# Optimization experiments

Measured on AMD Instinct MI355X. Metric: run time of the kernel, lower is better.

Reference implementation:

```python
import jax, jax.numpy as jnp
import numpy as np
from jax import lax

NMS_TH = 0.05
TOPK_P = 1000
NMS_IOU = 0.5
NUMDETS = 100
NMS_ITERS = 15
IM = 2048.0
SIZES = [256, 128, 64, 32, 16]
NUM_CLASS = 80


def _make_boxes(key, n):
    k1, k2, k3, k4 = jax.random.split(key, 4)
    cy = jax.random.uniform(k1, (n,)) * IM
    cx = jax.random.uniform(k2, (n,)) * IM
    h = jax.random.uniform(k3, (n,)) * 300.0 + 16.0
    w = jax.random.uniform(k4, (n,)) * 300.0 + 16.0
    # yxyx boxes
    return jnp.stack([cy - h / 2, cx - w / 2, cy + h / 2, cx + w / 2], axis=1)


def setup_inputs() -> dict:
    key = jax.random.key(0)
    inp = {}
    for s, sz in enumerate(SIZES):
        kc = jax.random.fold_in(key, 2 * s)
        kb = jax.random.fold_in(key, 2 * s + 1)
        n = sz * sz
        inp['cls%d' % s] = jax.random.normal(kc, (1, n, NUM_CLASS), jnp.float32) - 2.0
        inp['reg%d' % s] = _make_boxes(kb, n)[None]
    inp['locations'] = jnp.array([0.0, 0.0, IM - 1.0, IM - 1.0, 1024.0, 1024.0], jnp.float32)
    return inp


def _pairwise_iou(a, b):
    # a: (N,4) yxyx, b: (M,4) yxyx -> (N,M)
    area_a = jnp.clip(a[:, 2] - a[:, 0], 0) * jnp.clip(a[:, 3] - a[:, 1], 0)
    area_b = jnp.clip(b[:, 2] - b[:, 0], 0) * jnp.clip(b[:, 3] - b[:, 1], 0)
    iy1 = jnp.maximum(a[:, None, 0], b[None, :, 0])
    ix1 = jnp.maximum(a[:, None, 1], b[None, :, 1])
    iy2 = jnp.minimum(a[:, None, 2], b[None, :, 2])
    ix2 = jnp.minimum(a[:, None, 3], b[None, :, 3])
    inter = jnp.clip(iy2 - iy1, 0) * jnp.clip(ix2 - ix1, 0)
    union = area_a[:, None] + area_b[None, :] - inter
    return inter / jnp.maximum(union, 1e-9)


def _cluster_nms(boxes, scores, classes, valid, iou_th):
    order = jnp.argsort(-scores)
    b = boxes[order]
    s = scores[order]
    c = classes[order]
    v = valid[order]
    iou = jnp.triu(_pairwise_iou(b, b), k=1)  # (K,K)

    def body(B, _):
        max_a = B.max(axis=0)
        keep_col = (max_a <= iou_th).astype(B.dtype)[:, None]
        return iou * keep_col, None

    B, _ = lax.scan(body, iou, None, length=NMS_ITERS)
    keep = (B.max(axis=0) <= iou_th) & v
    return b, s, c, keep


def _per_level(cls_s, reg_s):
    p = jax.nn.sigmoid(cls_s[0])                 # (N, C)
    ps = p.max(axis=1)                           # (N,)
    pi = p.argmax(axis=1).astype(jnp.int32) + 1  # class index, 0 is background
    m = ps > NMS_TH
    ps_m = jnp.where(m, ps, -1.0)
    k = min(TOPK_P, ps_m.shape[0])
    top_s, top_idx = lax.top_k(ps_m, k)
    return top_s, pi[top_idx], reg_s[0][top_idx], m[top_idx]


def reference(cls0, cls1, cls2, cls3, cls4, reg0, reg1, reg2, reg3, reg4, locations):
    levels = [(cls0, reg0), (cls1, reg1), (cls2, reg2), (cls3, reg3), (cls4, reg4)]
    sc, cl, bx, vd = [], [], [], []
    for cls_s, reg_s in levels:
        s_, c_, b_, v_ = _per_level(cls_s, reg_s)
        sc.append(s_); cl.append(c_); bx.append(b_); vd.append(v_)
    scores = jnp.concatenate(sc)
    classes = jnp.concatenate(cl)
    boxes = jnp.concatenate(bx, axis=0)
    valid = jnp.concatenate(vd)
    scores = jnp.where(valid, scores, 0.0)

    vy1, vx1, vy2, vx2 = locations[0], locations[1], locations[2], locations[3]
    ori_h, ori_w = locations[4], locations[5]
    boxes = jnp.stack([
        jnp.maximum(boxes[:, 0], vy1), jnp.maximum(boxes[:, 1], vx1),
        jnp.minimum(boxes[:, 2], vy2), jnp.minimum(boxes[:, 3], vx2)], axis=1)

    b, s, c, keep = _cluster_nms(boxes, scores, classes, valid, NMS_IOU)
    s = jnp.where(keep, s, 0.0)
    top_s, sel = lax.top_k(s, NUMDETS)
    bbox = b[sel]
    cls_out = c[sel]

    # transfer boxes back to original-image coordinates
    sy = ori_h / jnp.maximum(vy2 - vy1, 1e-6)
    sx = ori_w / jnp.maximum(vx2 - vx1, 1e-6)
    bbox = jnp.stack([
        (bbox[:, 0] - vy1) * sy, (bbox[:, 1] - vx1) * sx,
        (bbox[:, 2] - vy1) * sy, (bbox[:, 3] - vx1) * sx], axis=1)
    return bbox, cls_out, top_s
```

## Files before the change

### kernel.cpp

```cpp
#include <hip/hip_runtime.h>
#include <math.h>


#define NANCH 87296
#define NF 4256
#define CAPD 128
#define NITER 16
#define BCAP 512
#define EC 8192
#define NBLK 341
#define BASE20 0xBD4CCu
#define NB20 9216
#define BPT 9

struct InPtrs {
    const float* cls[5];
    const float* reg[5];
    const float* loc;
};

constexpr size_t SZ_HIST  = 5ull * NB20 * 4;
constexpr size_t OFF_HIST = 0;
constexpr size_t OFF_CNT  = OFF_HIST + SZ_HIST;
constexpr size_t OFF_CTR  = OFF_CNT + (size_t)NF * 4;
constexpr size_t ZERO_SZ  = OFF_CTR + 128;
constexpr size_t OFF_SBITS = ((ZERO_SZ + 255) / 256) * 256;
constexpr size_t OFF_CLSV  = OFF_SBITS + (size_t)NANCH * 4;
constexpr size_t OFF_PAR   = OFF_CLSV + (size_t)NANCH * 4;
constexpr size_t OFF_INVB  = OFF_PAR + 128;
constexpr size_t OFF_INVO  = OFF_INVB + (size_t)NBLK * 4;
constexpr size_t OFF_FINK  = ((OFF_INVO + (size_t)NBLK * 4 + 255) / 256) * 256;
constexpr size_t OFF_BBUF  = OFF_FINK + (size_t)NF * 8;
constexpr size_t OFF_SBOX  = OFF_BBUF + 5ull * BCAP * 8;
constexpr size_t OFF_SSC   = OFF_SBOX + (size_t)NF * 16;
constexpr size_t OFF_SCV   = OFF_SSC + (size_t)NF * 4;
constexpr size_t OFF_SAR   = OFF_SCV + (size_t)NF * 4;
constexpr size_t OFF_NBR   = OFF_SAR + (size_t)NF * 4;

__device__ __forceinline__ void lvl_of(int a, int& lev, int& idx) {
    if (a < 65536)      { lev = 0; idx = a; }
    else if (a < 81920) { lev = 1; idx = a - 65536; }
    else if (a < 86016) { lev = 2; idx = a - 81920; }
    else if (a < 87040) { lev = 3; idx = a - 86016; }
    else                { lev = 4; idx = a - 87040; }
}

__device__ __forceinline__ unsigned int fkey(float f) {
    unsigned int u = __float_as_uint(f);
    return u ^ ((u & 0x80000000u) ? 0xFFFFFFFFu : 0x80000000u);
}
__device__ __forceinline__ float funkey(unsigned int k) {
    return __uint_as_float(k ^ ((k & 0x80000000u) ? 0x80000000u : 0xFFFFFFFFu));
}
__device__ __forceinline__ unsigned int bin20_addr(unsigned int v) {
    unsigned int owner = v / BPT;
    unsigned int i = v - owner * BPT;
    return (i << 10) | owner;
}
__device__ __forceinline__ unsigned int ald(const unsigned int* p) {
    return __hip_atomic_load((unsigned int*)p, __ATOMIC_RELAXED, __HIP_MEMORY_SCOPE_AGENT);
}
__device__ __forceinline__ void ast64(unsigned long long* p, unsigned long long v) {
    __hip_atomic_store(p, v, __ATOMIC_RELAXED, __HIP_MEMORY_SCOPE_AGENT);
}
__device__ __forceinline__ unsigned long long ald64(const unsigned long long* p) {
    return __hip_atomic_load((unsigned long long*)p, __ATOMIC_RELAXED, __HIP_MEMORY_SCOPE_AGENT);
}

__global__ __launch_bounds__(1024) void k1_score(InPtrs P, unsigned int* hist,
        unsigned int* sbits, unsigned int* clsv, unsigned int* invBlk) {
    int t = threadIdx.x;
    int a = blockIdx.x * 256 + (t >> 2);
    int k = t & 3;
    int lev, idx; lvl_of(a, lev, idx);
    const float4* row = (const float4*)(P.cls[lev] + (size_t)idx * 80);
    float4 v[5];
    #pragma unroll
    for (int q = 0; q < 5; ++q) v[q] = row[q * 4 + k];
    float best = -INFINITY; int bi = 0;
    #pragma unroll
    for (int q = 0; q < 5; ++q) {
        int c0 = q * 16 + k * 4;
        if (v[q].x > best) { best = v[q].x; bi = c0 + 0; }
        if (v[q].y > best) { best = v[q].y; bi = c0 + 1; }
        if (v[q].z > best) { best = v[q].z; bi = c0 + 2; }
        if (v[q].w > best) { best = v[q].w; bi = c0 + 3; }
    }
    #pragma unroll
    for (int m = 1; m < 4; m <<= 1) {
        float ob = __shfl_xor(best, m, 64);
        int  obi = __shfl_xor(bi, m, 64);
        if (ob > best || (ob == best && obi < bi)) { best = ob; bi = obi; }
    }
    bool lead = (k == 0);
    unsigned int valid = 0;
    if (lead) {
        float score = 1.0f / (1.0f + expf(-best));
        valid = (score > 0.05f) ? 1u : 0u;
        float psm = valid ? score : -1.0f;
        unsigned int sb = fkey(psm);
        sbits[a] = sb;
        clsv[a] = (unsigned int)(bi + 1) | (valid << 31);
        if (valid) {
            unsigned int bin = (sb >> 12) - BASE20;
            atomicAdd(&hist[(size_t)lev * NB20 + bin20_addr(bin)], 1u);
        }
    }
    __shared__ unsigned int wv[16];
    unsigned long long mv = __ballot(lead && valid);
    int lane = t & 63, w = t >> 6;
    if (lane == 0) wv[w] = (unsigned int)__popcll(mv);
    __syncthreads();
    if (t == 0) {
        unsigned int s = 0;
        #pragma unroll
        for (int i = 0; i < 16; ++i) s += wv[i];
        invBlk[blockIdx.x] = 256u - s;
    }
}

__global__ __launch_bounds__(1024) void k2_scan(const unsigned int* hist,
        const unsigned int* invBlk, unsigned int* params, unsigned int* invOff) {
    int t = threadIdx.x;
    if (blockIdx.x == 5) {
        __shared__ unsigned int sv[512];
        __shared__ unsigned int orig[512];
        if (t < 512) {
            unsigned int v = (t < NBLK) ? invBlk[t] : 0u;
            sv[t] = v; orig[t] = v;
        }
        __syncthreads();
        for (int off = 1; off < 512; off <<= 1) {
            unsigned int add = 0;
            if (t < 512 && t >= off) add = sv[t - off];
            __syncthreads();
            if (t < 512) sv[t] += add;
            __syncthreads();
        }
        if (t < NBLK) {
            int segStart = (t < 256) ? 0 : (t < 320) ? 256 : (t < 336) ? 320
                         : (t < 340) ? 336 : 340;
            invOff[t] = sv[t] - orig[t] - (segStart > 0 ? sv[segStart - 1] : 0u);
        }
        return;
    }
    int lev = blockIdx.x;
    unsigned int K = (lev == 4) ? 256u : 1000u;
    const unsigned int* h = hist + (size_t)lev * NB20;
    __shared__ unsigned int seg[1024];
    __shared__ unsigned int suf[1024];
    unsigned int hc[BPT];
    unsigned int s = 0;
    #pragma unroll
    for (int i = 0; i < BPT; ++i) { hc[i] = h[(i << 10) | t]; s += hc[i]; }
    seg[t] = s;
    suf[t] = s;
    __syncthreads();
    for (int off = 1; off < 1024; off <<= 1) {
        unsigned int v = suf[t];
        unsigned int add = (t + off < 1024) ? suf[t + off] : 0u;
        __syncthreads();
        suf[t] = v + add;
        __syncthreads();
    }
    unsigned int totValid = suf[0];
    if (totValid >= K) {
        unsigned int excl = suf[t] - seg[t];
        if (excl < K && excl + seg[t] >= K) {
            unsigned int cum = excl;
            for (int i = BPT - 1; i >= 0; --i) {
                unsigned int c = hc[i];
                if (cum + c >= K) {
                    params[lev] = (unsigned int)(t * BPT + i);
                    params[8 + lev] = K - cum;
                    params[16 + lev] = 0;
                    break;
                }
                cum += c;
            }
        }
    } else if (t == 0) {
        params[lev] = 0;
        params[8 + lev] = 0;
        params[16 + lev] = K - totValid;
    }
}

__global__ __launch_bounds__(256) void k3_compact(const unsigned int* sbits,
        const unsigned int* clsv, const unsigned int* params,
        const unsigned int* invOff, unsigned long long* finKeys,
        unsigned int* ctrs, unsigned long long* bBuf) {
    int blk = blockIdx.x;
    int t = threadIdx.x;
    int a = blk * 256 + t;
    int lev, idx; lvl_of(a, lev, idx);
    unsigned int sb = sbits[a];
    unsigned int cv = clsv[a];
    unsigned int bin = (sb >> 12) - BASE20;
    unsigned int Bs = params[lev];
    unsigned int rNeg = params[16 + lev];
    unsigned int valid = cv >> 31;
    int lane = t & 63, w = t >> 6;
    unsigned long long lt = (1ull << lane) - 1ull;
    __shared__ unsigned int wInv[4], wFin[4], wB[4];
    __shared__ unsigned int baseFin, baseB;
    unsigned long long mInv = __ballot(valid == 0u);
    if (lane == 0) wInv[w] = (unsigned int)__popcll(mInv);
    __syncthreads();
    unsigned int invRank = invOff[blk] + (unsigned int)__popcll(mInv & lt);
    for (int i = 0; i < w; ++i) invRank += wInv[i];
    bool isFin, isB;
    if (valid) {
        isFin = (bin > Bs);
        isB   = (bin == Bs);
    } else {
        isFin = (rNeg > 0) && (invRank < rNeg);
        isB   = false;
    }
    unsigned long long mFin = __ballot(isFin);
    unsigned long long mB   = __ballot(isB);
    if (lane == 0) { wFin[w] = (unsigned int)__popcll(mFin); wB[w] = (unsigned int)__popcll(mB); }
    __syncthreads();
    if (t == 0) {
        unsigned int tf = wFin[0] + wFin[1] + wFin[2] + wFin[3];
        unsigned int tb = wB[0] + wB[1] + wB[2] + wB[3];
        baseFin = tf ? atomicAdd(&ctrs[0], tf) : 0u;
        baseB   = tb ? atomicAdd(&ctrs[1 + lev], tb) : 0u;
    }
    __syncthreads();
    if (isFin || isB) {
        unsigned int composite = ((unsigned int)lev << 16) | (unsigned int)idx;
        unsigned int inv = (~composite) & 0x7FFFFu;
        unsigned int low = (inv << 13) | (valid << 7) | (cv & 0x7Fu);
        unsigned long long key = ((unsigned long long)sb << 32) | low;
        if (isFin) {
            unsigned int p = baseFin + (unsigned int)__popcll(mFin & lt);
            for (int i = 0; i < w; ++i) p += wFin[i];
            if (p < NF) finKeys[p] = key;
        } else {
            unsigned int p = baseB + (unsigned int)__popcll(mB & lt);
            for (int i = 0; i < w; ++i) p += wB[i];
            if (p < BCAP) ast64(&bBuf[(size_t)lev * BCAP + p], key);
        }
    }
    __shared__ unsigned int isLast;
    __shared__ unsigned long long kb[BCAP];
    __shared__ unsigned int posS;
    __syncthreads();
    if (t == 0) {
        asm volatile("s_waitcnt vmcnt(0)" ::: "memory");
        unsigned int r = __hip_atomic_fetch_add(&ctrs[8], 1u,
                             __ATOMIC_RELAXED, __HIP_MEMORY_SCOPE_AGENT);
        isLast = (r == (unsigned int)(NBLK - 1)) ? 1u : 0u;
    }
    __syncthreads();
    if (!isLast) return;
    unsigned int fc = ald(&ctrs[0]);
    if (fc > NF) fc = NF;
    if (t == 0) posS = fc;
    __syncthreads();
    for (int blev = 0; blev < 5; ++blev) {
        unsigned int bc = ald(&ctrs[1 + blev]);
        int n = (bc > BCAP) ? BCAP : (int)bc;
        int r = (int)params[8 + blev];
        if (r > n) r = n;
        if (r > 0) {
            for (int i = t; i < n; i += 256)
                kb[i] = ald64(&bBuf[(size_t)blev * BCAP + i]);
            __syncthreads();
            for (int i = t; i < n; i += 256) {
                unsigned long long my = kb[i];
                unsigned int c = 0;
                for (int j = 0; j < n; ++j) c += (kb[j] > my) ? 1u : 0u;
                if (c < (unsigned int)r) {
                    unsigned int p = atomicAdd(&posS, 1u);
                    if (p < NF) finKeys[p] = my;
                }
            }
            __syncthreads();
        }
    }
    for (int i = (int)posS + t; i < NF; i += 256)
        finKeys[i] = (unsigned long long)i;
}

__global__ __launch_bounds__(1024) void k5_rank(InPtrs P,
        const unsigned long long* finKeys,
        float4* sBox, float* sScore, unsigned int* sCV, float* sArea) {
    __shared__ __align__(16) unsigned long long keys[NF];
    __shared__ unsigned int rnk[64];
    int t = threadIdx.x;
    {
        const ulonglong2* src = (const ulonglong2*)finKeys;
        ulonglong2* dst = (ulonglong2*)keys;
        for (int i = t; i < NF / 2; i += 1024) dst[i] = src[i];
    }
    if (t < 64) rnk[t] = 0;
    __syncthreads();
    int lf = t & 63;
    int seg = t >> 6;
    int f = blockIdx.x * 64 + lf;
    unsigned long long my = (f < NF) ? keys[f] : 0ull;
    if (f < NF) {
        unsigned int c = 0;
        const ulonglong2* kp = (const ulonglong2*)keys + seg * 133;
        #pragma unroll 4
        for (int i = 0; i < 133; ++i) {
            ulonglong2 v = kp[i];
            c += (v.x > my) ? 1u : 0u;
            c += (v.y > my) ? 1u : 0u;
        }
        atomicAdd(&rnk[lf], c);
    }
    __syncthreads();
    if (seg == 0 && f < NF) {
        unsigned int r = rnk[lf];
        unsigned int sb  = (unsigned int)(my >> 32);
        unsigned int low = (unsigned int)my;
        unsigned int composite = (~(low >> 13)) & 0x7FFFFu;
        int lev = composite >> 16;
        int idx = composite & 0xFFFF;
        float4 b = ((const float4*)P.reg[lev])[idx];
        float vy1 = P.loc[0], vx1 = P.loc[1], vy2 = P.loc[2], vx2 = P.loc[3];
        float y1 = fmaxf(b.x, vy1), x1 = fmaxf(b.y, vx1);
        float y2 = fminf(b.z, vy2), x2 = fminf(b.w, vx2);
        float area = __fmul_rn(fmaxf(y2 - y1, 0.0f), fmaxf(x2 - x1, 0.0f));
        unsigned int valid = (low >> 7) & 1u;
        sBox[r] = make_float4(y1, x1, y2, x2);
        sScore[r] = valid ? funkey(sb) : 0.0f;
        sCV[r] = (low & 0x7Fu) | (valid << 31);
        sArea[r] = area;
    }
}

__global__ __launch_bounds__(256) void k6_adj(const float4* sBox,
        const float* sArea, unsigned int* cnt, unsigned short* nbr) {
    int L = blockIdx.x;
    float fr = sqrtf(8.0f * (float)L + 1.0f);
    int jt = (int)((fr - 1.0f) * 0.5f);
    while ((jt + 1) * (jt + 2) / 2 <= L) jt++;
    while (jt * (jt + 1) / 2 > L) jt--;
    int it = L - jt * (jt + 1) / 2;
    __shared__ float4 cb[64]; __shared__ float ca[64];
    __shared__ float4 rb[64]; __shared__ float ra[64];
    int t = threadIdx.x;
    if (t < 64) {
        int j = jt * 64 + t;
        if (j < NF) { cb[t] = sBox[j]; ca[t] = sArea[j]; }
        int i = it * 64 + t;
        if (i < NF) { rb[t] = sBox[i]; ra[t] = sArea[i]; }
    }
    __syncthreads();
    int lj = t & 63;
    int j = jt * 64 + lj;
    if (j >= NF) return;
    float4 B = cb[lj]; float ab = ca[lj];
    for (int li = (t >> 6); li < 64; li += 4) {
        int i = it * 64 + li;
        if (i >= j) continue;
        float4 A = rb[li]; float aa = ra[li];
        float iy1 = fmaxf(A.x, B.x), ix1 = fmaxf(A.y, B.y);
        float iy2 = fminf(A.z, B.z), ix2 = fminf(A.w, B.w);
        float ih = fmaxf(iy2 - iy1, 0.0f), iw = fmaxf(ix2 - ix1, 0.0f);
        float inter = __fmul_rn(ih, iw);
        float uni = __fsub_rn(__fadd_rn(aa, ab), inter);
        float iou = __fdiv_rn(inter, fmaxf(uni, 1e-9f));
        if (iou > 0.5f) {
            unsigned int p = atomicAdd(&cnt[j], 1u);
            if (p < CAPD) nbr[(size_t)j * CAPD + p] = (unsigned short)i;
        }
    }
}

__global__ __launch_bounds__(1024) void k7_nms(InPtrs P, const float4* sBox,
        const float* sScore, const unsigned int* sCV, const unsigned int* cnt,
        const unsigned short* nbr, float* out) {
    __shared__ unsigned int edges[EC];
    __shared__ __align__(4) unsigned char bufA[NF];
    __shared__ __align__(4) unsigned char bufB[NF];
    __shared__ unsigned int wsum[16];
    __shared__ float ploc[6];
    __shared__ unsigned int chg;
    int t = threadIdx.x;
    int lane = t & 63, wid = t >> 6;
    if (t < 6) ploc[t] = P.loc[t];
    const int CH = 5;
    unsigned int dq[CH];
    unsigned int s = 0;
    #pragma unroll
    for (int q = 0; q < CH; ++q) {
        int j = t * CH + q;
        unsigned int d = 0;
        if (j < NF) { d = cnt[j]; if (d > CAPD) d = CAPD; }
        dq[q] = d; s += d;
    }
    unsigned int sc = s;
    #pragma unroll
    for (int o = 1; o < 64; o <<= 1) {
        unsigned int n = __shfl_up(sc, o, 64);
        if (lane >= o) sc += n;
    }
    if (lane == 63) wsum[wid] = sc;
    if (t < 1064) ((unsigned int*)bufA)[t] = 0x01010101u;
    __syncthreads();
    unsigned int wbase = 0, tot = 0;
    #pragma unroll
    for (int i = 0; i < 16; ++i) {
        unsigned int v = wsum[i];
        if (i < wid) wbase += v;
        tot += v;
    }
    unsigned int E = tot;
    bool useLds = (E <= (unsigned int)EC);
    if (useLds) {
        unsigned int base = wbase + sc - s;
        #pragma unroll
        for (int q = 0; q < CH; ++q) {
            int j = t * CH + q;
            if (j < NF) {
                unsigned int d = dq[q];
                const unsigned short* nl = nbr + (size_t)j * CAPD;
                for (unsigned int e = 0; e < d; ++e)
                    edges[base + e] = ((unsigned int)nl[e] << 16) | (unsigned int)j;
                base += d;
            }
        }
    }
    __syncthreads();
    unsigned char* cur = bufA; unsigned char* nxt = bufB;
    for (int itr = 0; itr < NITER; ++itr) {
        if (t < 1064) ((unsigned int*)nxt)[t] = 0x01010101u;
        __syncthreads();
        if (useLds) {
            for (int e = t; e < (int)E; e += 1024) {
                unsigned int pk = edges[e];
                if (cur[pk >> 16]) nxt[pk & 0xFFFFu] = 0;
            }
        } else {
            for (int j = t; j < NF; j += 1024) {
                unsigned int d = cnt[j]; if (d > CAPD) d = CAPD;
                const unsigned short* nl = nbr + (size_t)j * CAPD;
                unsigned int hit = 0;
                for (unsigned int e = 0; e < d; ++e)
                    hit |= (unsigned int)cur[nl[e]];
                if (hit) nxt[j] = 0;
            }
        }
        __syncthreads();
        if (t < 1064 &&
            ((unsigned int*)nxt)[t] != ((unsigned int*)cur)[t]) chg = 1;
        __syncthreads();
        unsigned int done = (chg == 0u);
        unsigned char* tm = cur; cur = nxt; nxt = tm;
        __syncthreads();
        if (t == 0) chg = 0;
        if (done) break;
    }
    int base = t * CH;
    unsigned char kf[CH];
    unsigned int sum = 0;
    #pragma unroll
    for (int q = 0; q < CH; ++q) {
        int j = base + q;
        unsigned char v = 0;
        if (j < NF) v = cur[j] & (unsigned char)(sCV[j] >> 31);
        kf[q] = v; sum += v;
    }
    unsigned int sc2 = sum;
    #pragma unroll
    for (int o = 1; o < 64; o <<= 1) {
        unsigned int n = __shfl_up(sc2, o, 64);
        if (lane >= o) sc2 += n;
    }
    if (lane == 63) wsum[wid] = sc2;
    __syncthreads();
    unsigned int wbase2 = 0, keptTot = 0;
    #pragma unroll
    for (int i = 0; i < 16; ++i) {
        unsigned int v = wsum[i];
        if (i < wid) wbase2 += v;
        keptTot += v;
    }
    unsigned int run = wbase2 + sc2 - sum;
    float vy1 = ploc[0], vx1 = ploc[1], vy2 = ploc[2], vx2 = ploc[3];
    float sy = ploc[4] / fmaxf(vy2 - vy1, 1e-6f);
    float sx = ploc[5] / fmaxf(vx2 - vx1, 1e-6f);
    #pragma unroll
    for (int q = 0; q < CH; ++q) {
        int j = base + q;
        if (j >= NF) break;
        unsigned int slot = 0xFFFFFFFFu;
        float scv = 0.0f;
        if (kf[q]) {
            if (run < 100u) { slot = run; scv = sScore[j]; }
            run++;
        } else if (keptTot < 100u) {
            unsigned int nk = (unsigned int)j - run;
            unsigned int s2 = keptTot + nk;
            if (s2 < 100u) { slot = s2; scv = 0.0f; }
        }
        if (slot < 100u) {
            float4 b = sBox[j];
            out[slot * 4 + 0] = (b.x - vy1) * sy;
            out[slot * 4 + 1] = (b.y - vx1) * sx;
            out[slot * 4 + 2] = (b.z - vy1) * sy;
            out[slot * 4 + 3] = (b.w - vx1) * sx;
            out[400 + slot] = (float)(sCV[j] & 0x7Fu);
            out[500 + slot] = scv;
        }
    }
}

extern "C" void kernel_launch(void* const* d_in, const int* in_sizes, int n_in,
                              void* d_out, int out_size, void* d_ws, size_t ws_size,
                              hipStream_t stream) {
    (void)n_in; (void)out_size; (void)ws_size;
    InPtrs P;
    bool inter = (in_sizes[1] == 65536 * 4);
    for (int s = 0; s < 5; ++s) {
        P.cls[s] = (const float*)d_in[inter ? 2 * s : s];
        P.reg[s] = (const float*)d_in[inter ? 2 * s + 1 : 5 + s];
    }
    P.loc = (const float*)d_in[10];

    char* w = (char*)d_ws;
    unsigned int* hist   = (unsigned int*)(w + OFF_HIST);
    unsigned int* cnt    = (unsigned int*)(w + OFF_CNT);
    unsigned int* ctrs   = (unsigned int*)(w + OFF_CTR);
    unsigned int* sbits  = (unsigned int*)(w + OFF_SBITS);
    unsigned int* clsv   = (unsigned int*)(w + OFF_CLSV);
    unsigned int* params = (unsigned int*)(w + OFF_PAR);
    unsigned int* invBlk = (unsigned int*)(w + OFF_INVB);
    unsigned int* invOff = (unsigned int*)(w + OFF_INVO);
    unsigned long long* finKeys = (unsigned long long*)(w + OFF_FINK);
    unsigned long long* bBuf    = (unsigned long long*)(w + OFF_BBUF);
    float4* sBox  = (float4*)(w + OFF_SBOX);
    float* sScore = (float*)(w + OFF_SSC);
    unsigned int* sCV = (unsigned int*)(w + OFF_SCV);
    float* sArea  = (float*)(w + OFF_SAR);
    unsigned short* nbr = (unsigned short*)(w + OFF_NBR);

    hipMemsetAsync(d_ws, 0, ZERO_SZ, stream);
    k1_score<<<NBLK, 1024, 0, stream>>>(P, hist, sbits, clsv, invBlk);
    k2_scan<<<6, 1024, 0, stream>>>(hist, invBlk, params, invOff);
    k3_compact<<<NBLK, 256, 0, stream>>>(sbits, clsv, params, invOff, finKeys, ctrs, bBuf);
    k5_rank<<<67, 1024, 0, stream>>>(P, finKeys, sBox, sScore, sCV, sArea);
    k6_adj<<<2278, 256, 0, stream>>>(sBox, sArea, cnt, nbr);
    k7_nms<<<1, 1024, 0, stream>>>(P, sBox, sScore, sCV, cnt, nbr, (float*)d_out);
}
```

Measured before the change: 173.0 us.

## Fuse scan into score kernel and rank into compact kernel via last-block patterns

Removes two kernel launches. The histogram threshold scan and invalid-offset scan now run in the last block to finish k1_score, found with an atomic counter. The rank stage is folded into the compact kernel: the last 67 blocks to arrive spin-wait on a flag set by the final block after it has merged the boundary-bin keys, then each computes ranks with 256 threads instead of 1024. This cuts launch gaps but makes blocks busy-wait inside the grid and narrows the rank parallelism per block.

Result: slower. 192.0 us (+11.0%).

```diff
diff --git a/kernel.cpp b/kernel.cpp
--- a/kernel.cpp
+++ b/kernel.cpp
@@ -12,6 +12,7 @@
 #define BASE20 0xBD4CCu
 #define NB20 9216
 #define BPT 9
+#define NRANK 67
 
 struct InPtrs {
     const float* cls[5];
@@ -60,6 +61,9 @@
 __device__ __forceinline__ unsigned int ald(const unsigned int* p) {
     return __hip_atomic_load((unsigned int*)p, __ATOMIC_RELAXED, __HIP_MEMORY_SCOPE_AGENT);
 }
+__device__ __forceinline__ void ast(unsigned int* p, unsigned int v) {
+    __hip_atomic_store(p, v, __ATOMIC_RELAXED, __HIP_MEMORY_SCOPE_AGENT);
+}
 __device__ __forceinline__ void ast64(unsigned long long* p, unsigned long long v) {
     __hip_atomic_store(p, v, __ATOMIC_RELAXED, __HIP_MEMORY_SCOPE_AGENT);
 }
@@ -68,7 +72,8 @@
 }
 
 __global__ __launch_bounds__(1024) void k1_score(InPtrs P, unsigned int* hist,
-        unsigned int* sbits, unsigned int* clsv, unsigned int* invBlk) {
+        unsigned int* sbits, unsigned int* clsv, unsigned int* invBlk,
+        unsigned int* params, unsigned int* invOff, unsigned int* ctrs) {
     int t = threadIdx.x;
     int a = blockIdx.x * 256 + (t >> 2);
     int k = t & 3;
@@ -107,6 +112,7 @@
         }
     }
     __shared__ unsigned int wv[16];
+    __shared__ unsigned int isLast;
     unsigned long long mv = __ballot(lead && valid);
     int lane = t & 63, w = t >> 6;
     if (lane == 0) wv[w] = (unsigned int)__popcll(mv);
@@ -115,81 +121,91 @@
         unsigned int s = 0;
         #pragma unroll
         for (int i = 0; i < 16; ++i) s += wv[i];
-        invBlk[blockIdx.x] = 256u - s;
-    }
-}
-
-__global__ __launch_bounds__(1024) void k2_scan(const unsigned int* hist,
-        const unsigned int* invBlk, unsigned int* params, unsigned int* invOff) {
-    int t = threadIdx.x;
-    if (blockIdx.x == 5) {
-        __shared__ unsigned int sv[512];
-        __shared__ unsigned int orig[512];
-        if (t < 512) {
-            unsigned int v = (t < NBLK) ? invBlk[t] : 0u;
-            sv[t] = v; orig[t] = v;
-        }
-        __syncthreads();
-        for (int off = 1; off < 512; off <<= 1) {
-            unsigned int add = 0;
-            if (t < 512 && t >= off) add = sv[t - off];
-            __syncthreads();
-            if (t < 512) sv[t] += add;
-            __syncthreads();
-        }
-        if (t < NBLK) {
-            int segStart = (t < 256) ? 0 : (t < 320) ? 256 : (t < 336) ? 320
-                         : (t < 340) ? 336 : 340;
-            invOff[t] = sv[t] - orig[t] - (segStart > 0 ? sv[segStart - 1] : 0u);
-        }
-        return;
-    }
-    int lev = blockIdx.x;
-    unsigned int K = (lev == 4) ? 256u : 1000u;
-    const unsigned int* h = hist + (size_t)lev * NB20;
-    __shared__ unsigned int seg[1024];
-    __shared__ unsigned int suf[1024];
-    unsigned int hc[BPT];
-    unsigned int s = 0;
-    #pragma unroll
-    for (int i = 0; i < BPT; ++i) { hc[i] = h[(i << 10) | t]; s += hc[i]; }
-    seg[t] = s;
-    suf[t] = s;
+        ast(&invBlk[blockIdx.x], 256u - s);
+    }
+    __syncthreads();
+    if (t == 0) {
+        asm volatile("s_waitcnt vmcnt(0)" ::: "memory");
+        unsigned int r = __hip_atomic_fetch_add(&ctrs[11], 1u,
+                             __ATOMIC_RELAXED, __HIP_MEMORY_SCOPE_AGENT);
+        isLast = (r == (unsigned int)(NBLK - 1)) ? 1u : 0u;
+    }
+    __syncthreads();
+    if (!isLast) return;
+
+    __shared__ unsigned int sc[5 * 1024];
+    unsigned int s4[5];
+    #pragma unroll
+    for (int lv = 0; lv < 5; ++lv) {
+        const unsigned int* h = hist + (size_t)lv * NB20;
+        unsigned int s = 0;
+        #pragma unroll
+        for (int i = 0; i < BPT; ++i) s += ald(&h[(i << 10) | t]);
+        s4[lv] = s; sc[lv * 1024 + t] = s;
+    }
     __syncthreads();
     for (int off = 1; off < 1024; off <<= 1) {
-        unsigned int v = suf[t];
-        unsigned int add = (t + off < 1024) ? suf[t + off] : 0u;
-        __syncthreads();
-        suf[t] = v + add;
-        __syncthreads();
-    }
-    unsigned int totValid = suf[0];
-    if (totValid >= K) {
-        unsigned int excl = suf[t] - seg[t];
-        if (excl < K && excl + seg[t] >= K) {
-            unsigned int cum = excl;
-            for (int i = BPT - 1; i >= 0; --i) {
-                unsigned int c = hc[i];
-                if (cum + c >= K) {
-                    params[lev] = (unsigned int)(t * BPT + i);
-                    params[8 + lev] = K - cum;
-                    params[16 + lev] = 0;
-                    break;
+        unsigned int vv[5], a2[5];
+        #pragma unroll
+        for (int lv = 0; lv < 5; ++lv) {
+            vv[lv] = sc[lv * 1024 + t];
+            a2[lv] = (t + off < 1024) ? sc[lv * 1024 + t + off] : 0u;
+        }
+        __syncthreads();
+        #pragma unroll
+        for (int lv = 0; lv < 5; ++lv) sc[lv * 1024 + t] = vv[lv] + a2[lv];
+        __syncthreads();
+    }
+    #pragma unroll
+    for (int lv = 0; lv < 5; ++lv) {
+        unsigned int K = (lv == 4) ? 256u : 1000u;
+        unsigned int tot = sc[lv * 1024];
+        if (tot >= K) {
+            unsigned int suf = sc[lv * 1024 + t];
+            unsigned int excl = suf - s4[lv];
+            if (excl < K && suf >= K) {
+                const unsigned int* h = hist + (size_t)lv * NB20;
+                unsigned int cum = excl;
+                for (int i = BPT - 1; i >= 0; --i) {
+                    unsigned int c = ald(&h[(i << 10) | t]);
+                    if (cum + c >= K) {
+                        params[lv] = (unsigned int)(t * BPT + i);
+                        params[8 + lv] = K - cum;
+                        params[16 + lv] = 0;
+                        break;
+                    }
+                    cum += c;
                 }
-                cum += c;
             }
-        }
-    } else if (t == 0) {
-        params[lev] = 0;
-        params[8 + lev] = 0;
-        params[16 + lev] = K - totValid;
-    }
-}
-
-__global__ __launch_bounds__(256) void k3_compact(const unsigned int* sbits,
-        const unsigned int* clsv, const unsigned int* params,
-        const unsigned int* invOff, unsigned long long* finKeys,
-        unsigned int* ctrs, unsigned long long* bBuf) {
+        } else if (t == 0) {
+            params[lv] = 0; params[8 + lv] = 0; params[16 + lv] = K - tot;
+        }
+    }
+    __syncthreads();
+    if (t < 512) {
+        unsigned int vv = (t < NBLK) ? ald(&invBlk[t]) : 0u;
+        sc[t] = vv; sc[1024 + t] = vv;
+    }
+    __syncthreads();
+    for (int off = 1; off < 512; off <<= 1) {
+        unsigned int add = 0;
+        if (t < 512 && t >= off) add = sc[t - off];
+        __syncthreads();
+        if (t < 512) sc[t] += add;
+        __syncthreads();
+    }
+    if (t < NBLK) {
+        int segStart = (t < 256) ? 0 : (t < 320) ? 256 : (t < 336) ? 320
+                     : (t < 340) ? 336 : 340;
+        invOff[t] = sc[t] - sc[1024 + t] - (segStart > 0 ? sc[segStart - 1] : 0u);
+    }
+}
+
+__global__ __launch_bounds__(256) void k3_rank(InPtrs P,
+        const unsigned int* sbits, const unsigned int* clsv,
+        const unsigned int* params, const unsigned int* invOff,
+        unsigned long long* finKeys, unsigned int* ctrs, unsigned long long* bBuf,
+        float4* sBox, float* sScore, unsigned int* sCV, float* sArea) {
     int blk = blockIdx.x;
     int t = threadIdx.x;
     int a = blk * 256 + t;
@@ -203,23 +219,23 @@
     int lane = t & 63, w = t >> 6;
     unsigned long long lt = (1ull << lane) - 1ull;
     __shared__ unsigned int wInv[4], wFin[4], wB[4];
-    __shared__ unsigned int baseFin, baseB;
+    __shared__ unsigned int baseFin, baseB, myRank, posS;
+    __shared__ union {
+        unsigned long long kb[BCAP];
+        struct { unsigned long long keys[NF]; unsigned int rnk[64]; } rk;
+    } u;
     unsigned long long mInv = __ballot(valid == 0u);
     if (lane == 0) wInv[w] = (unsigned int)__popcll(mInv);
     __syncthreads();
     unsigned int invRank = invOff[blk] + (unsigned int)__popcll(mInv & lt);
     for (int i = 0; i < w; ++i) invRank += wInv[i];
     bool isFin, isB;
-    if (valid) {
-        isFin = (bin > Bs);
-        isB   = (bin == Bs);
-    } else {
-        isFin = (rNeg > 0) && (invRank < rNeg);
-        isB   = false;
-    }
+    if (valid) { isFin = (bin > Bs); isB = (bin == Bs); }
+    else       { isFin = (rNeg > 0) && (invRank < rNeg); isB = false; }
     unsigned long long mFin = __ballot(isFin);
     unsigned long long mB   = __ballot(isB);
-    if (lane == 0) { wFin[w] = (unsigned int)__popcll(mFin); wB[w] = (unsigned int)__popcll(mB); }
+    if (lane == 0) { wFin[w] = (unsigned int)__popcll(mFin);
+                     wB[w]   = (unsigned int)__popcll(mB); }
     __syncthreads();
     if (t == 0) {
         unsigned int tf = wFin[0] + wFin[1] + wFin[2] + wFin[3];
@@ -236,99 +252,97 @@
         if (isFin) {
             unsigned int p = baseFin + (unsigned int)__popcll(mFin & lt);
             for (int i = 0; i < w; ++i) p += wFin[i];
-            if (p < NF) finKeys[p] = key;
+            if (p < NF) ast64(&finKeys[p], key);
         } else {
             unsigned int p = baseB + (unsigned int)__popcll(mB & lt);
             for (int i = 0; i < w; ++i) p += wB[i];
             if (p < BCAP) ast64(&bBuf[(size_t)lev * BCAP + p], key);
         }
     }
-    __shared__ unsigned int isLast;
-    __shared__ unsigned long long kb[BCAP];
-    __shared__ unsigned int posS;
     __syncthreads();
     if (t == 0) {
         asm volatile("s_waitcnt vmcnt(0)" ::: "memory");
-        unsigned int r = __hip_atomic_fetch_add(&ctrs[8], 1u,
-                             __ATOMIC_RELAXED, __HIP_MEMORY_SCOPE_AGENT);
-        isLast = (r == (unsigned int)(NBLK - 1)) ? 1u : 0u;
-    }
-    __syncthreads();
-    if (!isLast) return;
-    unsigned int fc = ald(&ctrs[0]);
-    if (fc > NF) fc = NF;
-    if (t == 0) posS = fc;
-    __syncthreads();
-    for (int blev = 0; blev < 5; ++blev) {
-        unsigned int bc = ald(&ctrs[1 + blev]);
-        int n = (bc > BCAP) ? BCAP : (int)bc;
-        int r = (int)params[8 + blev];
-        if (r > n) r = n;
-        if (r > 0) {
-            for (int i = t; i < n; i += 256)
-                kb[i] = ald64(&bBuf[(size_t)blev * BCAP + i]);
-            __syncthreads();
-            for (int i = t; i < n; i += 256) {
-                unsigned long long my = kb[i];
-                unsigned int c = 0;
-                for (int j = 0; j < n; ++j) c += (kb[j] > my) ? 1u : 0u;
-                if (c < (unsigned int)r) {
-                    unsigned int p = atomicAdd(&posS, 1u);
-                    if (p < NF) finKeys[p] = my;
+        myRank = __hip_atomic_fetch_add(&ctrs[8], 1u,
+                     __ATOMIC_RELAXED, __HIP_MEMORY_SCOPE_AGENT);
+    }
+    __syncthreads();
+    unsigned int rk_ = myRank;
+    if (rk_ < (unsigned int)(NBLK - 1 - NRANK)) return;
+
+    if (rk_ == (unsigned int)(NBLK - 1)) {
+        unsigned int fc = ald(&ctrs[0]);
+        if (fc > NF) fc = NF;
+        if (t == 0) posS = fc;
+        __syncthreads();
+        for (int blev = 0; blev < 5; ++blev) {
+            unsigned int bc = ald(&ctrs[1 + blev]);
+            int n = (bc > BCAP) ? BCAP : (int)bc;
+            int r = (int)params[8 + blev];
+            if (r > n) r = n;
+            if (r > 0) {
+                for (int i = t; i < n; i += 256)
+                    u.kb[i] = ald64(&bBuf[(size_t)blev * BCAP + i]);
+                __syncthreads();
+                for (int i = t; i < n; i += 256) {
+                    unsigned long long my = u.kb[i];
+                    unsigned int c = 0;
+                    for (int j = 0; j < n; ++j) c += (u.kb[j] > my) ? 1u : 0u;
+                    if (c < (unsigned int)r) {
+                        unsigned int p = atomicAdd(&posS, 1u);
+                        if (p < NF) ast64(&finKeys[p], my);
+                    }
                 }
+                __syncthreads();
             }
-            __syncthreads();
-        }
-    }
-    for (int i = (int)posS + t; i < NF; i += 256)
-        finKeys[i] = (unsigned long long)i;
-}
-
-__global__ __launch_bounds__(1024) void k5_rank(InPtrs P,
-        const unsigned long long* finKeys,
-        float4* sBox, float* sScore, unsigned int* sCV, float* sArea) {
-    __shared__ __align__(16) unsigned long long keys[NF];
-    __shared__ unsigned int rnk[64];
-    int t = threadIdx.x;
-    {
-        const ulonglong2* src = (const ulonglong2*)finKeys;
-        ulonglong2* dst = (ulonglong2*)keys;
-        for (int i = t; i < NF / 2; i += 1024) dst[i] = src[i];
-    }
-    if (t < 64) rnk[t] = 0;
+        }
+        __syncthreads();
+        for (int i = (int)posS + t; i < NF; i += 256)
+            ast64(&finKeys[i], (unsigned long long)i);
+        __syncthreads();
+        if (t == 0) {
+            asm volatile("s_waitcnt vmcnt(0)" ::: "memory");
+            ast(&ctrs[10], 1u);
+        }
+        return;
+    }
+
+    if (t == 0) {
+        int g = 0;
+        while (ald(&ctrs[10]) == 0u && g < 200000) { __builtin_amdgcn_s_sleep(8); ++g; }
+    }
+    __syncthreads();
+    int rb = (int)rk_ - (NBLK - 1 - NRANK);
+    for (int i = t; i < NF; i += 256) u.rk.keys[i] = ald64(&finKeys[i]);
+    if (t < 64) u.rk.rnk[t] = 0;
     __syncthreads();
     int lf = t & 63;
     int seg = t >> 6;
-    int f = blockIdx.x * 64 + lf;
-    unsigned long long my = (f < NF) ? keys[f] : 0ull;
+    int f = rb * 64 + lf;
+    unsigned long long my = (f < NF) ? u.rk.keys[f] : 0ull;
     if (f < NF) {
         unsigned int c = 0;
-        const ulonglong2* kp = (const ulonglong2*)keys + seg * 133;
-        #pragma unroll 4
-        for (int i = 0; i < 133; ++i) {
-            ulonglong2 v = kp[i];
-            c += (v.x > my) ? 1u : 0u;
-            c += (v.y > my) ? 1u : 0u;
-        }
-        atomicAdd(&rnk[lf], c);
+        const unsigned long long* kp = u.rk.keys + seg * 1064;
+        #pragma unroll 8
+        for (int i = 0; i < 1064; ++i) c += (kp[i] > my) ? 1u : 0u;
+        atomicAdd(&u.rk.rnk[lf], c);
     }
     __syncthreads();
     if (seg == 0 && f < NF) {
-        unsigned int r = rnk[lf];
-        unsigned int sb  = (unsigned int)(my >> 32);
+        unsigned int r = u.rk.rnk[lf];
+        unsigned int sbv = (unsigned int)(my >> 32);
         unsigned int low = (unsigned int)my;
         unsigned int composite = (~(low >> 13)) & 0x7FFFFu;
-        int lev = composite >> 16;
-        int idx = composite & 0xFFFF;
-        float4 b = ((const float4*)P.reg[lev])[idx];
+        int lev2 = composite >> 16;
+        int idx2 = composite & 0xFFFF;
+        float4 b = ((const float4*)P.reg[lev2])[idx2];
         float vy1 = P.loc[0], vx1 = P.loc[1], vy2 = P.loc[2], vx2 = P.loc[3];
         float y1 = fmaxf(b.x, vy1), x1 = fmaxf(b.y, vx1);
         float y2 = fminf(b.z, vy2), x2 = fminf(b.w, vx2);
         float area = __fmul_rn(fmaxf(y2 - y1, 0.0f), fmaxf(x2 - x1, 0.0f));
-        unsigned int valid = (low >> 7) & 1u;
+        unsigned int valid2 = (low >> 7) & 1u;
         sBox[r] = make_float4(y1, x1, y2, x2);
-        sScore[r] = valid ? funkey(sb) : 0.0f;
-        sCV[r] = (low & 0x7Fu) | (valid << 31);
+        sScore[r] = valid2 ? funkey(sbv) : 0.0f;
+        sCV[r] = (low & 0x7Fu) | (valid2 << 31);
         sArea[r] = area;
     }
 }
@@ -541,10 +555,10 @@
     unsigned short* nbr = (unsigned short*)(w + OFF_NBR);
 
     hipMemsetAsync(d_ws, 0, ZERO_SZ, stream);
-    k1_score<<<NBLK, 1024, 0, stream>>>(P, hist, sbits, clsv, invBlk);
-    k2_scan<<<6, 1024, 0, stream>>>(hist, invBlk, params, invOff);
-    k3_compact<<<NBLK, 256, 0, stream>>>(sbits, clsv, params, invOff, finKeys, ctrs, bBuf);
-    k5_rank<<<67, 1024, 0, stream>>>(P, finKeys, sBox, sScore, sCV, sArea);
+    k1_score<<<NBLK, 1024, 0, stream>>>(P, hist, sbits, clsv, invBlk,
+                                        params, invOff, ctrs);
+    k3_rank<<<NBLK, 256, 0, stream>>>(P, sbits, clsv, params, invOff,
+                                      finKeys, ctrs, bBuf, sBox, sScore, sCV, sArea);
     k6_adj<<<2278, 256, 0, stream>>>(sBox, sArea, cnt, nbr);
     k7_nms<<<1, 1024, 0, stream>>>(P, sBox, sScore, sCV, cnt, nbr, (float*)d_out);
 }
```
